# Optimization experiments

Measured on AMD Instinct MI355X. Metric: run time of the kernel, lower is better.

The kernel has to match this reference:

```python
import jax, jax.numpy as jnp
import numpy as np

B, T, D = 2, 2048, 1024
N, H = 16, 64  # num_heads, head_dim
LOG2E = 1.442695041
NEG_INF = -1.0e9


def setup_inputs() -> dict:
    key = jax.random.key(0)
    ks = jax.random.split(key, 6)
    return {
        "input_tensor": jax.random.normal(ks[0], (B, T, D), dtype=jnp.float32),
        "attention_mask": jax.random.randint(ks[1], (B, 1, T, T), 0, 2, dtype=jnp.int32),
        "wq": jax.random.normal(ks[2], (D, N, H), dtype=jnp.float32),
        "bq": jnp.zeros((N, H), dtype=jnp.float32),
        "wk": jax.random.normal(ks[3], (D, N, H), dtype=jnp.float32),
        "bk": jnp.zeros((N, H), dtype=jnp.float32),
        "wv": jax.random.normal(ks[4], (D, N, H), dtype=jnp.float32),
        "bv": jnp.zeros((N, H), dtype=jnp.float32),
        "wo": jax.random.normal(ks[5], (D, N, H), dtype=jnp.float32),
        "bo": jnp.zeros((D,), dtype=jnp.float32),
        "per_dim_scale": jnp.zeros((H,), dtype=jnp.float32),
    }


def reference(input_tensor, attention_mask, wq, bq, wk, bk, wv, bv, wo, bo, per_dim_scale):
    # QKV projections: [B,T,D] x [D,N,H] -> [B,T,N,H]
    q = jnp.einsum('btd,dnh->btnh', input_tensor, wq) + bq
    k = jnp.einsum('btd,dnh->btnh', input_tensor, wk) + bk
    v = jnp.einsum('btd,dnh->btnh', input_tensor, wv) + bv
    # per-dim query scaling: (log2(e)/sqrt(H)) * softplus(per_dim_scale)
    scale = (LOG2E / jnp.sqrt(jnp.asarray(H, q.dtype))) * jax.nn.softplus(per_dim_scale)
    q = q * scale
    # scores: [B,N,T,S]
    scores = jnp.einsum('btnh,bsnh->bnts', q, k)
    scores = jnp.where(attention_mask == 0, jnp.asarray(NEG_INF, scores.dtype), scores)
    weights = jax.nn.softmax(scores, axis=-1)
    # AV: [B,N,T,S] x [B,S,N,H] -> [B,T,N,H]
    attn_out = jnp.einsum('bnts,bsnh->btnh', weights, v)
    # output projection: [B,T,N,H] x [D,N,H] -> [B,T,D]
    return jnp.einsum('btnh,dnh->btd', attn_out, wo) + bo
```

## Files before the change

kernel.cpp:

```cpp
#include <hip/hip_runtime.h>
#include <math.h>

typedef __bf16 bf16;
typedef __attribute__((ext_vector_type(8))) __bf16 bf16x8;
typedef __attribute__((ext_vector_type(4))) __bf16 bf16x4;
typedef __attribute__((ext_vector_type(4))) float f32x4;

#define BB 2
#define TT 2048
#define DD 1024
#define NHD 16
#define HD 64
#define MM (BB*TT)
#define LOG2E_F 1.442695041f
#define NEGINF_F (-1.0e9f)

__device__ __forceinline__ void gld16(const bf16* g, bf16* l)
{
    __builtin_amdgcn_global_load_lds(
        (const __attribute__((address_space(1))) unsigned int*)g,
        (__attribute__((address_space(3))) unsigned int*)l, 16, 0, 0);
}

__global__ __launch_bounds__(256)
void prep_all(const float* __restrict__ X, const int* __restrict__ m,
              const float* __restrict__ wq, const float* __restrict__ wk,
              const float* __restrict__ wv, const float* __restrict__ wo,
              bf16* __restrict__ Xh, bf16* __restrict__ Xl,
              bf16* __restrict__ qkh, bf16* __restrict__ qkl,
              bf16* __restrict__ vh, bf16* __restrict__ ob,
              unsigned* __restrict__ bits)
{
    __shared__ float tile[32][33];
    const int bid = blockIdx.x;
    const int t   = threadIdx.x;

    if (bid < 4096) {
        int i = bid * 256 + t;
        float4 v = ((const float4*)X)[i];
        float f[4] = {v.x, v.y, v.z, v.w};
        bf16x4 h, l;
        #pragma unroll
        for (int j = 0; j < 4; ++j) {
            bf16 hh = (bf16)f[j];
            h[j] = hh;
            l[j] = (bf16)(f[j] - (float)hh);
        }
        *(bf16x4*)(Xh + (size_t)i * 4) = h;
        *(bf16x4*)(Xl + (size_t)i * 4) = l;
        return;
    }
    if (bid < 8192) {
        const int idx = bid - 4096;
        const int z   = idx >> 10;
        const int bx  = (idx & 31) << 5;
        const int by  = ((idx >> 5) & 31) << 5;
        const int r   = t >> 3;
        const int c4  = (t & 7) << 2;
        if (z == 3) {
            float4 v = *(const float4*)(wo + (size_t)(by + r) * 1024 + bx + c4);
            bf16x4 o = { (bf16)v.x, (bf16)v.y, (bf16)v.z, (bf16)v.w };
            *(bf16x4*)(ob + (size_t)(by + r) * 1024 + bx + c4) = o;
            return;
        }
        const float* src = (z == 0) ? wq : ((z == 1) ? wk : wv);
        bf16* oh = (z == 0) ? qkh : ((z == 1) ? qkh + 1048576 : vh);
        bf16* ol = (z == 0) ? qkl : ((z == 1) ? qkl + 1048576 : nullptr);
        float4 v = *(const float4*)(src + (size_t)(by + r) * 1024 + bx + c4);
        tile[r][c4+0] = v.x; tile[r][c4+1] = v.y;
        tile[r][c4+2] = v.z; tile[r][c4+3] = v.w;
        __syncthreads();
        bf16x4 hv, lv;
        #pragma unroll
        for (int j = 0; j < 4; ++j) {
            float f = tile[c4 + j][r];
            bf16 h = (bf16)f;
            hv[j] = h;
            lv[j] = (bf16)(f - (float)h);
        }
        *(bf16x4*)(oh + (size_t)(bx + r) * 1024 + by + c4) = hv;
        if (ol)
            *(bf16x4*)(ol + (size_t)(bx + r) * 1024 + by + c4) = lv;
        return;
    }
    {
        int i = (bid - 8192) * 256 + t;
        int lane = t & 63;
        int v = m[i];
        unsigned long long bl = __ballot(v != 0);
        if ((lane & 31) == 0)
            bits[i >> 5] = (unsigned)(bl >> (lane & 32));
    }
}

__global__ __launch_bounds__(256)
void gemm_qk(const bf16* __restrict__ Xh, const bf16* __restrict__ Xl,
             const bf16* __restrict__ Wh, const bf16* __restrict__ Wl,
             const float* __restrict__ bq, const float* __restrict__ bk,
             const float* __restrict__ pds,
             bf16* __restrict__ oQh, bf16* __restrict__ oQl,
             bf16* __restrict__ oKh, bf16* __restrict__ oKl)
{
    __shared__ bf16 Ah[128 * 32];
    __shared__ bf16 Al[128 * 32];
    __shared__ bf16 Bh[128 * 32];
    __shared__ bf16 Bl[128 * 32];

    const int t    = threadIdx.x;
    const int lane = t & 63;
    const int w    = t >> 6;
    const int quad = lane >> 4, l15 = lane & 15;
    const int m0   = blockIdx.y << 7;
    const int n0   = blockIdx.x << 7;
    const int wm   = (w >> 1) << 6;
    const int wn   = (w & 1)  << 6;

    const int jr0 = ((w * 2 + 0) << 4) + (lane >> 2);
    const int jr1 = ((w * 2 + 1) << 4) + (lane >> 2);
    const int kch = (lane & 3) << 3;

    bf16* lAh0 = Ah + (w * 2 + 0) * 512;  bf16* lAh1 = Ah + (w * 2 + 1) * 512;
    bf16* lAl0 = Al + (w * 2 + 0) * 512;  bf16* lAl1 = Al + (w * 2 + 1) * 512;
    bf16* lBh0 = Bh + (w * 2 + 0) * 512;  bf16* lBh1 = Bh + (w * 2 + 1) * 512;
    bf16* lBl0 = Bl + (w * 2 + 0) * 512;  bf16* lBl1 = Bl + (w * 2 + 1) * 512;

    const bf16* pAh0 = Xh + (size_t)(m0 + jr0) * DD + kch;
    const bf16* pAh1 = Xh + (size_t)(m0 + jr1) * DD + kch;
    const bf16* pAl0 = Xl + (size_t)(m0 + jr0) * DD + kch;
    const bf16* pAl1 = Xl + (size_t)(m0 + jr1) * DD + kch;
    const bf16* pBh0 = Wh + (size_t)(n0 + jr0) * DD + kch;
    const bf16* pBh1 = Wh + (size_t)(n0 + jr1) * DD + kch;
    const bf16* pBl0 = Wl + (size_t)(n0 + jr0) * DD + kch;
    const bf16* pBl1 = Wl + (size_t)(n0 + jr1) * DD + kch;

    f32x4 acc[4][4] = {};

    for (int k0 = 0; k0 < DD; k0 += 32) {
        __syncthreads();
        gld16(pAh0 + k0, lAh0);  gld16(pAh1 + k0, lAh1);
        gld16(pAl0 + k0, lAl0);  gld16(pAl1 + k0, lAl1);
        gld16(pBh0 + k0, lBh0);  gld16(pBh1 + k0, lBh1);
        gld16(pBl0 + k0, lBl0);  gld16(pBl1 + k0, lBl1);
        __syncthreads();

        bf16x8 ah[4], bh[4];
        #pragma unroll
        for (int mt = 0; mt < 4; ++mt)
            ah[mt] = *(const bf16x8*)(Ah + (wm + (mt << 4) + l15) * 32 + (quad << 3));
        #pragma unroll
        for (int nt = 0; nt < 4; ++nt)
            bh[nt] = *(const bf16x8*)(Bh + (wn + (nt << 4) + l15) * 32 + (quad << 3));
        #pragma unroll
        for (int mt = 0; mt < 4; ++mt)
            #pragma unroll
            for (int nt = 0; nt < 4; ++nt)
                acc[mt][nt] = __builtin_amdgcn_mfma_f32_16x16x32_bf16(
                    ah[mt], bh[nt], acc[mt][nt], 0, 0, 0);

        bf16x8 bl[4];
        #pragma unroll
        for (int nt = 0; nt < 4; ++nt)
            bl[nt] = *(const bf16x8*)(Bl + (wn + (nt << 4) + l15) * 32 + (quad << 3));
        #pragma unroll
        for (int mt = 0; mt < 4; ++mt)
            #pragma unroll
            for (int nt = 0; nt < 4; ++nt)
                acc[mt][nt] = __builtin_amdgcn_mfma_f32_16x16x32_bf16(
                    ah[mt], bl[nt], acc[mt][nt], 0, 0, 0);

        bf16x8 al[4];
        #pragma unroll
        for (int mt = 0; mt < 4; ++mt)
            al[mt] = *(const bf16x8*)(Al + (wm + (mt << 4) + l15) * 32 + (quad << 3));
        #pragma unroll
        for (int mt = 0; mt < 4; ++mt)
            #pragma unroll
            for (int nt = 0; nt < 4; ++nt)
                acc[mt][nt] = __builtin_amdgcn_mfma_f32_16x16x32_bf16(
                    al[mt], bh[nt], acc[mt][nt], 0, 0, 0);
    }

    #pragma unroll
    for (int nt = 0; nt < 4; ++nt) {
        const int col = n0 + wn + (nt << 4) + l15;
        const int isQ = (col < 1024);
        const int nh  = col & 1023;
        const int n   = nh >> 6, h = nh & 63;
        const float bcol = isQ ? bq[nh] : bk[nh];
        float s = 1.f;
        if (isQ) {
            float x  = pds[h];
            float sp = fmaxf(x, 0.f) + log1pf(expf(-fabsf(x)));
            s = (LOG2E_F * LOG2E_F / 8.0f) * sp;
        }
        bf16* dH = isQ ? oQh : oKh;
        bf16* dL = isQ ? oQl : oKl;
        #pragma unroll
        for (int mt = 0; mt < 4; ++mt) {
            #pragma unroll
            for (int reg = 0; reg < 4; ++reg) {
                const int row = m0 + wm + (mt << 4) + (quad << 2) + reg;
                const int bi  = row >> 11;
                const int tt  = row & (TT - 1);
                float val = (acc[mt][nt][reg] + bcol) * s;
                const size_t idx = (((size_t)bi * NHD + n) * TT + tt) * HD + h;
                bf16 hi = (bf16)val;
                dH[idx] = hi;
                dL[idx] = (bf16)(val - (float)hi);
            }
        }
    }
}

__global__ __launch_bounds__(256)
void gemm128(const bf16* __restrict__ A, const bf16* __restrict__ Bt,
             const float* __restrict__ bias,
             bf16* __restrict__ oVt, float* __restrict__ oF, const int mode)
{
    __shared__ bf16 As[128 * 32];
    __shared__ bf16 Bs[128 * 32];

    const int t    = threadIdx.x;
    const int lane = t & 63;
    const int w    = t >> 6;
    const int quad = lane >> 4, l15 = lane & 15;
    const int m0   = blockIdx.y << 7;
    const int n0   = blockIdx.x << 7;
    const int wm   = (w >> 1) << 6;
    const int wn   = (w & 1)  << 6;

    const int jr0 = ((w * 2 + 0) << 4) + (lane >> 2);
    const int jr1 = ((w * 2 + 1) << 4) + (lane >> 2);
    const int kch = (lane & 3) << 3;

    bf16* lA0 = As + (w * 2 + 0) * 512;
    bf16* lA1 = As + (w * 2 + 1) * 512;
    bf16* lB0 = Bs + (w * 2 + 0) * 512;
    bf16* lB1 = Bs + (w * 2 + 1) * 512;

    const bf16* Ap0 = A  + (size_t)(m0 + jr0) * DD + kch;
    const bf16* Ap1 = A  + (size_t)(m0 + jr1) * DD + kch;
    const bf16* Bp0 = Bt + (size_t)(n0 + jr0) * DD + kch;
    const bf16* Bp1 = Bt + (size_t)(n0 + jr1) * DD + kch;

    f32x4 acc[4][4] = {};

    for (int k0 = 0; k0 < DD; k0 += 32) {
        __syncthreads();
        gld16(Ap0 + k0, lA0);
        gld16(Ap1 + k0, lA1);
        gld16(Bp0 + k0, lB0);
        gld16(Bp1 + k0, lB1);
        __syncthreads();
        bf16x8 af[4], bfm[4];
        #pragma unroll
        for (int mt = 0; mt < 4; ++mt)
            af[mt] = *(const bf16x8*)(As + (wm + (mt << 4) + l15) * 32 + (quad << 3));
        #pragma unroll
        for (int nt = 0; nt < 4; ++nt)
            bfm[nt] = *(const bf16x8*)(Bs + (wn + (nt << 4) + l15) * 32 + (quad << 3));
        #pragma unroll
        for (int mt = 0; mt < 4; ++mt)
            #pragma unroll
            for (int nt = 0; nt < 4; ++nt)
                acc[mt][nt] = __builtin_amdgcn_mfma_f32_16x16x32_bf16(
                    af[mt], bfm[nt], acc[mt][nt], 0, 0, 0);
    }

    if (mode == 1) {
        #pragma unroll
        for (int nt = 0; nt < 4; ++nt) {
            const int col = n0 + wn + (nt << 4) + l15;
            const int bi  = col >> 11;
            const int tt  = col & (TT - 1);
            #pragma unroll
            for (int mt = 0; mt < 4; ++mt) {
                #pragma unroll
                for (int reg = 0; reg < 4; ++reg) {
                    const int row = m0 + wm + (mt << 4) + (quad << 2) + reg;
                    float val = acc[mt][nt][reg] + bias[row];
                    oVt[((size_t)bi * 1024 + row) * TT + tt] = (bf16)val;
                }
            }
        }
    } else {
        #pragma unroll
        for (int nt = 0; nt < 4; ++nt) {
            const int col = n0 + wn + (nt << 4) + l15;
            const float bcol = bias[col];
            #pragma unroll
            for (int mt = 0; mt < 4; ++mt) {
                #pragma unroll
                for (int reg = 0; reg < 4; ++reg) {
                    const int row = m0 + wm + (mt << 4) + (quad << 2) + reg;
                    oF[(size_t)row * DD + col] = acc[mt][nt][reg] + bcol;
                }
            }
        }
    }
}

__global__ __launch_bounds__(256)
void attn_mfma(const bf16* __restrict__ Qh, const bf16* __restrict__ Ql,
               const bf16* __restrict__ Kh, const bf16* __restrict__ Kl,
               const bf16* __restrict__ Vt, const unsigned* __restrict__ mbits,
               bf16* __restrict__ AO)
{
    __shared__ bf16 Ksh[64][72];
    __shared__ bf16 Ksl[64][72];
    __shared__ bf16 Vts[64][72];
    __shared__ bf16 Ps[4][16][72];
    __shared__ unsigned msk[64][2];

    const int t    = threadIdx.x;
    const int lane = t & 63;
    const int w    = t >> 6;
    const int quad = lane >> 4, l15 = lane & 15;
    const int bn   = blockIdx.y;
    const int b    = bn >> 4, n = bn & 15;
    const int q0   = blockIdx.x << 6;

    const bf16* Qbh = Qh + (size_t)bn * TT * HD;
    const bf16* Qbl = Ql + (size_t)bn * TT * HD;
    const bf16* Kbh = Kh + (size_t)bn * TT * HD;
    const bf16* Kbl = Kl + (size_t)bn * TT * HD;
    const bf16* Vtb = Vt + (size_t)bn * HD * TT;

    const int qrow = q0 + (w << 4) + l15;
    bf16x8 qfh[2], qfl[2];
    qfh[0] = *(const bf16x8*)(Qbh + (size_t)qrow * HD + (quad << 3));
    qfh[1] = *(const bf16x8*)(Qbh + (size_t)qrow * HD + 32 + (quad << 3));
    qfl[0] = *(const bf16x8*)(Qbl + (size_t)qrow * HD + (quad << 3));
    qfl[1] = *(const bf16x8*)(Qbl + (size_t)qrow * HD + 32 + (quad << 3));

    f32x4 O[4];
    #pragma unroll
    for (int i = 0; i < 4; ++i) O[i] = (f32x4){0.f,0.f,0.f,0.f};
    float m_i = -INFINITY;
    float l_i = 0.f;

    const int rS = t >> 2, cS = (t & 3) << 4;

    for (int kb = 0; kb < TT; kb += 64) {
        const bf16* kph = Kbh + (size_t)(kb + rS) * HD + cS;
        const bf16* kpl = Kbl + (size_t)(kb + rS) * HD + cS;
        bf16x8 kh0 = *(const bf16x8*)kph;
        bf16x8 kh1 = *(const bf16x8*)(kph + 8);
        bf16x8 kl0 = *(const bf16x8*)kpl;
        bf16x8 kl1 = *(const bf16x8*)(kpl + 8);
        const bf16* vp = Vtb + (size_t)rS * TT + kb + cS;
        bf16x8 v0v = *(const bf16x8*)vp;
        bf16x8 v1v = *(const bf16x8*)(vp + 8);
        unsigned mw = 0;
        if (t < 128)
            mw = mbits[((size_t)b * TT + q0 + (t >> 1)) * (TT / 32) + (kb >> 5) + (t & 1)];

        __syncthreads();
        *(bf16x8*)&Ksh[rS][cS]     = kh0;
        *(bf16x8*)&Ksh[rS][cS + 8] = kh1;
        *(bf16x8*)&Ksl[rS][cS]     = kl0;
        *(bf16x8*)&Ksl[rS][cS + 8] = kl1;
        *(bf16x8*)&Vts[rS][cS]     = v0v;
        *(bf16x8*)&Vts[rS][cS + 8] = v1v;
        if (t < 128) msk[t >> 1][t & 1] = mw;
        __syncthreads();

        f32x4 s_acc[4];
        #pragma unroll
        for (int i = 0; i < 4; ++i) s_acc[i] = (f32x4){0.f,0.f,0.f,0.f};
        #pragma unroll
        for (int k2 = 0; k2 < 2; ++k2) {
            #pragma unroll
            for (int nt = 0; nt < 4; ++nt) {
                bf16x8 bkh = *(const bf16x8*)&Ksh[(nt << 4) + l15][(k2 << 5) + (quad << 3)];
                bf16x8 bkl = *(const bf16x8*)&Ksl[(nt << 4) + l15][(k2 << 5) + (quad << 3)];
                s_acc[nt] = __builtin_amdgcn_mfma_f32_16x16x32_bf16(bkh, qfh[k2], s_acc[nt], 0, 0, 0);
                s_acc[nt] = __builtin_amdgcn_mfma_f32_16x16x32_bf16(bkl, qfh[k2], s_acc[nt], 0, 0, 0);
                s_acc[nt] = __builtin_amdgcn_mfma_f32_16x16x32_bf16(bkh, qfl[k2], s_acc[nt], 0, 0, 0);
            }
        }

        const unsigned w0 = msk[(w << 4) + l15][0];
        const unsigned w1 = msk[(w << 4) + l15][1];
        float sv[16];
        #pragma unroll
        for (int nt = 0; nt < 4; ++nt) {
            const unsigned word = (nt & 2) ? w1 : w0;
            #pragma unroll
            for (int reg = 0; reg < 4; ++reg) {
                const int bit = ((nt & 1) << 4) + (quad << 2) + reg;
                sv[nt * 4 + reg] = ((word >> bit) & 1u) ? s_acc[nt][reg] : NEGINF_F;
            }
        }
        float mx = sv[0];
        #pragma unroll
        for (int i = 1; i < 16; ++i) mx = fmaxf(mx, sv[i]);
        mx = fmaxf(mx, __shfl_xor(mx, 16));
        mx = fmaxf(mx, __shfl_xor(mx, 32));
        const float mnew  = fmaxf(m_i, mx);
        const float alpha = exp2f(m_i - mnew);
        float p[16], sum = 0.f;
        #pragma unroll
        for (int i = 0; i < 16; ++i) { p[i] = exp2f(sv[i] - mnew); sum += p[i]; }
        sum += __shfl_xor(sum, 16);
        sum += __shfl_xor(sum, 32);
        l_i = l_i * alpha + sum;
        m_i = mnew;
        #pragma unroll
        for (int nt = 0; nt < 4; ++nt) {
            O[nt][0] *= alpha; O[nt][1] *= alpha;
            O[nt][2] *= alpha; O[nt][3] *= alpha;
            bf16x4 pv = { (bf16)p[nt * 4 + 0], (bf16)p[nt * 4 + 1],
                          (bf16)p[nt * 4 + 2], (bf16)p[nt * 4 + 3] };
            *(bf16x4*)&Ps[w][l15][(nt << 4) + (quad << 2)] = pv;
        }

        #pragma unroll
        for (int s2 = 0; s2 < 2; ++s2) {
            bf16x8 ap = *(const bf16x8*)&Ps[w][l15][(s2 << 5) + (quad << 3)];
            #pragma unroll
            for (int nt = 0; nt < 4; ++nt) {
                bf16x8 bv = *(const bf16x8*)&Vts[(nt << 4) + l15][(s2 << 5) + (quad << 3)];
                O[nt] = __builtin_amdgcn_mfma_f32_16x16x32_bf16(bv, ap, O[nt], 0, 0, 0);
            }
        }
    }

    {
        const float inv = 1.0f / l_i;
        const size_t base = ((size_t)b * TT + qrow) * (NHD * HD) + (size_t)n * HD;
        #pragma unroll
        for (int nt = 0; nt < 4; ++nt) {
            bf16x4 o = { (bf16)(O[nt][0] * inv), (bf16)(O[nt][1] * inv),
                         (bf16)(O[nt][2] * inv), (bf16)(O[nt][3] * inv) };
            *(bf16x4*)(AO + base + (nt << 4) + (quad << 2)) = o;
        }
    }
}

extern "C" void kernel_launch(void* const* d_in, const int* in_sizes, int n_in,
                              void* d_out, int out_size, void* d_ws, size_t ws_size,
                              hipStream_t stream)
{
    const float* X   = (const float*)d_in[0];
    const int*   msk = (const int*)d_in[1];
    const float* wq  = (const float*)d_in[2];
    const float* bq  = (const float*)d_in[3];
    const float* wk  = (const float*)d_in[4];
    const float* bk  = (const float*)d_in[5];
    const float* wv  = (const float*)d_in[6];
    const float* bv  = (const float*)d_in[7];
    const float* wo  = (const float*)d_in[8];
    const float* bo  = (const float*)d_in[9];
    const float* pds = (const float*)d_in[10];
    float* out = (float*)d_out;

    bf16* ws   = (bf16*)d_ws;
    bf16* Xh   = ws;
    bf16* Xl   = ws + 4194304;
    bf16* WQKh = ws + 8388608;
    bf16* WQKl = ws + 10485760;
    bf16* Wvh  = ws + 12582912;
    bf16* Wob  = ws + 13631488;
    bf16* Qhb  = ws + 14680064;
    bf16* Qlb  = ws + 18874368;
    bf16* Khb  = ws + 23068672;
    bf16* Klb  = ws + 27262976;
    unsigned* mbits = (unsigned*)(ws + 31457280);
    bf16* Vtb  = Xl;
    bf16* AOb  = Xh;

    dim3 blk(256);

    prep_all<<<40960, blk, 0, stream>>>(X, msk, wq, wk, wv, wo,
                                        Xh, Xl, WQKh, WQKl, Wvh, Wob, mbits);

    gemm_qk<<<dim3(16, 32), blk, 0, stream>>>(
        Xh, Xl, WQKh, WQKl, bq, bk, pds, Qhb, Qlb, Khb, Klb);

    gemm128<<<dim3(32, 8), blk, 0, stream>>>(
        Wvh, Xh, bv, Vtb, nullptr, 1);

    dim3 ga(TT / 64, BB * NHD);
    attn_mfma<<<ga, blk, 0, stream>>>(Qhb, Qlb, Khb, Klb, Vtb, mbits, AOb);

    gemm128<<<dim3(8, 32), blk, 0, stream>>>(
        AOb, Wob, bo, nullptr, out, 2);
}
```

Measured before the change: 344.5 us.

## Merge QK and V projection launches and double attention query tile to 128

Combines the Q/K split-precision projection and the V projection into a single kernel launch dispatched by block index, writing V to a separate workspace region so the two are independent. Attention blocks now use 512 threads covering 128 query rows, halving repeated K/V and Vt tile loads per query. This trades fewer, larger attention blocks and possibly lower occupancy for less launch overhead and more shared-memory reuse.

```diff
diff --git a/kernel.cpp b/kernel.cpp
--- a/kernel.cpp
+++ b/kernel.cpp
@@ -94,17 +94,181 @@
 }
 
 __global__ __launch_bounds__(256)
-void gemm_qk(const bf16* __restrict__ Xh, const bf16* __restrict__ Xl,
-             const bf16* __restrict__ Wh, const bf16* __restrict__ Wl,
-             const float* __restrict__ bq, const float* __restrict__ bk,
-             const float* __restrict__ pds,
-             bf16* __restrict__ oQh, bf16* __restrict__ oQl,
-             bf16* __restrict__ oKh, bf16* __restrict__ oKl)
+void gemm_proj(const bf16* __restrict__ Xh, const bf16* __restrict__ Xl,
+               const bf16* __restrict__ Wh, const bf16* __restrict__ Wl,
+               const bf16* __restrict__ Wvh,
+               const float* __restrict__ bq, const float* __restrict__ bk,
+               const float* __restrict__ bv, const float* __restrict__ pds,
+               bf16* __restrict__ oQh, bf16* __restrict__ oQl,
+               bf16* __restrict__ oKh, bf16* __restrict__ oKl,
+               bf16* __restrict__ oVt)
 {
-    __shared__ bf16 Ah[128 * 32];
-    __shared__ bf16 Al[128 * 32];
-    __shared__ bf16 Bh[128 * 32];
-    __shared__ bf16 Bl[128 * 32];
+    __shared__ bf16 S[4][128 * 32];
+
+    const int bid  = blockIdx.x;
+    const int t    = threadIdx.x;
+    const int lane = t & 63;
+    const int w    = t >> 6;
+    const int quad = lane >> 4, l15 = lane & 15;
+    const int wm   = (w >> 1) << 6;
+    const int wn   = (w & 1)  << 6;
+
+    const int jr0 = ((w * 2 + 0) << 4) + (lane >> 2);
+    const int jr1 = ((w * 2 + 1) << 4) + (lane >> 2);
+    const int kch = (lane & 3) << 3;
+    const int off0 = (w * 2 + 0) * 512;
+    const int off1 = (w * 2 + 1) * 512;
+
+    if (bid < 512) {
+        const int m0 = (bid >> 4) << 7;
+        const int n0 = (bid & 15) << 7;
+        bf16* Ah = S[0]; bf16* Al = S[1]; bf16* Bh = S[2]; bf16* Bl = S[3];
+
+        const bf16* pAh0 = Xh + (size_t)(m0 + jr0) * DD + kch;
+        const bf16* pAh1 = Xh + (size_t)(m0 + jr1) * DD + kch;
+        const bf16* pAl0 = Xl + (size_t)(m0 + jr0) * DD + kch;
+        const bf16* pAl1 = Xl + (size_t)(m0 + jr1) * DD + kch;
+        const bf16* pBh0 = Wh + (size_t)(n0 + jr0) * DD + kch;
+        const bf16* pBh1 = Wh + (size_t)(n0 + jr1) * DD + kch;
+        const bf16* pBl0 = Wl + (size_t)(n0 + jr0) * DD + kch;
+        const bf16* pBl1 = Wl + (size_t)(n0 + jr1) * DD + kch;
+
+        f32x4 acc[4][4] = {};
+
+        for (int k0 = 0; k0 < DD; k0 += 32) {
+            __syncthreads();
+            gld16(pAh0 + k0, Ah + off0);  gld16(pAh1 + k0, Ah + off1);
+            gld16(pAl0 + k0, Al + off0);  gld16(pAl1 + k0, Al + off1);
+            gld16(pBh0 + k0, Bh + off0);  gld16(pBh1 + k0, Bh + off1);
+            gld16(pBl0 + k0, Bl + off0);  gld16(pBl1 + k0, Bl + off1);
+            __syncthreads();
+
+            bf16x8 ah[4], bh[4];
+            #pragma unroll
+            for (int mt = 0; mt < 4; ++mt)
+                ah[mt] = *(const bf16x8*)(Ah + (wm + (mt << 4) + l15) * 32 + (quad << 3));
+            #pragma unroll
+            for (int nt = 0; nt < 4; ++nt)
+                bh[nt] = *(const bf16x8*)(Bh + (wn + (nt << 4) + l15) * 32 + (quad << 3));
+            #pragma unroll
+            for (int mt = 0; mt < 4; ++mt)
+                #pragma unroll
+                for (int nt = 0; nt < 4; ++nt)
+                    acc[mt][nt] = __builtin_amdgcn_mfma_f32_16x16x32_bf16(
+                        ah[mt], bh[nt], acc[mt][nt], 0, 0, 0);
+
+            bf16x8 bl[4];
+            #pragma unroll
+            for (int nt = 0; nt < 4; ++nt)
+                bl[nt] = *(const bf16x8*)(Bl + (wn + (nt << 4) + l15) * 32 + (quad << 3));
+            #pragma unroll
+            for (int mt = 0; mt < 4; ++mt)
+                #pragma unroll
+                for (int nt = 0; nt < 4; ++nt)
+                    acc[mt][nt] = __builtin_amdgcn_mfma_f32_16x16x32_bf16(
+                        ah[mt], bl[nt], acc[mt][nt], 0, 0, 0);
+
+            bf16x8 al[4];
+            #pragma unroll
+            for (int mt = 0; mt < 4; ++mt)
+                al[mt] = *(const bf16x8*)(Al + (wm + (mt << 4) + l15) * 32 + (quad << 3));
+            #pragma unroll
+            for (int mt = 0; mt < 4; ++mt)
+                #pragma unroll
+                for (int nt = 0; nt < 4; ++nt)
+                    acc[mt][nt] = __builtin_amdgcn_mfma_f32_16x16x32_bf16(
+                        al[mt], bh[nt], acc[mt][nt], 0, 0, 0);
+        }
+
+        #pragma unroll
+        for (int nt = 0; nt < 4; ++nt) {
+            const int col = n0 + wn + (nt << 4) + l15;
+            const int isQ = (col < 1024);
+            const int nh  = col & 1023;
+            const int n   = nh >> 6, h = nh & 63;
+            const float bcol = isQ ? bq[nh] : bk[nh];
+            float s = 1.f;
+            if (isQ) {
+                float x  = pds[h];
+                float sp = fmaxf(x, 0.f) + log1pf(expf(-fabsf(x)));
+                s = (LOG2E_F * LOG2E_F / 8.0f) * sp;
+            }
+            bf16* dH = isQ ? oQh : oKh;
+            bf16* dL = isQ ? oQl : oKl;
+            #pragma unroll
+            for (int mt = 0; mt < 4; ++mt) {
+                #pragma unroll
+                for (int reg = 0; reg < 4; ++reg) {
+                    const int row = m0 + wm + (mt << 4) + (quad << 2) + reg;
+                    const int bi  = row >> 11;
+                    const int tt  = row & (TT - 1);
+                    float val = (acc[mt][nt][reg] + bcol) * s;
+                    const size_t idx = (((size_t)bi * NHD + n) * TT + tt) * HD + h;
+                    bf16 hi = (bf16)val;
+                    dH[idx] = hi;
+                    dL[idx] = (bf16)(val - (float)hi);
+                }
+            }
+        }
+    } else {
+        const int idx = bid - 512;
+        const int m0  = (idx >> 5) << 7;
+        const int n0  = (idx & 31) << 7;
+        bf16* As = S[0]; bf16* Bs = S[2];
+
+        const bf16* Ap0 = Wvh + (size_t)(m0 + jr0) * DD + kch;
+        const bf16* Ap1 = Wvh + (size_t)(m0 + jr1) * DD + kch;
+        const bf16* Bp0 = Xh  + (size_t)(n0 + jr0) * DD + kch;
+        const bf16* Bp1 = Xh  + (size_t)(n0 + jr1) * DD + kch;
+
+        f32x4 acc[4][4] = {};
+
+        for (int k0 = 0; k0 < DD; k0 += 32) {
+            __syncthreads();
+            gld16(Ap0 + k0, As + off0);
+            gld16(Ap1 + k0, As + off1);
+            gld16(Bp0 + k0, Bs + off0);
+            gld16(Bp1 + k0, Bs + off1);
+            __syncthreads();
+            bf16x8 af[4], bfm[4];
+            #pragma unroll
+            for (int mt = 0; mt < 4; ++mt)
+                af[mt] = *(const bf16x8*)(As + (wm + (mt << 4) + l15) * 32 + (quad << 3));
+            #pragma unroll
+            for (int nt = 0; nt < 4; ++nt)
+                bfm[nt] = *(const bf16x8*)(Bs + (wn + (nt << 4) + l15) * 32 + (quad << 3));
+            #pragma unroll
+            for (int mt = 0; mt < 4; ++mt)
+                #pragma unroll
+                for (int nt = 0; nt < 4; ++nt)
+                    acc[mt][nt] = __builtin_amdgcn_mfma_f32_16x16x32_bf16(
+                        af[mt], bfm[nt], acc[mt][nt], 0, 0, 0);
+        }
+
+        #pragma unroll
+        for (int nt = 0; nt < 4; ++nt) {
+            const int col = n0 + wn + (nt << 4) + l15;
+            const int bi  = col >> 11;
+            const int tt  = col & (TT - 1);
+            #pragma unroll
+            for (int mt = 0; mt < 4; ++mt) {
+                #pragma unroll
+                for (int reg = 0; reg < 4; ++reg) {
+                    const int row = m0 + wm + (mt << 4) + (quad << 2) + reg;
+                    float val = acc[mt][nt][reg] + bv[row];
+                    oVt[((size_t)bi * 1024 + row) * TT + tt] = (bf16)val;
+                }
+            }
+        }
+    }
+}
+
+__global__ __launch_bounds__(256)
+void gemm_out(const bf16* __restrict__ A, const bf16* __restrict__ Bt,
+              const float* __restrict__ bias, float* __restrict__ oF)
+{
+    __shared__ bf16 As[128 * 32];
+    __shared__ bf16 Bs[128 * 32];
 
     const int t    = threadIdx.x;
     const int lane = t & 63;
@@ -119,120 +283,6 @@
     const int jr1 = ((w * 2 + 1) << 4) + (lane >> 2);
     const int kch = (lane & 3) << 3;
 
-    bf16* lAh0 = Ah + (w * 2 + 0) * 512;  bf16* lAh1 = Ah + (w * 2 + 1) * 512;
-    bf16* lAl0 = Al + (w * 2 + 0) * 512;  bf16* lAl1 = Al + (w * 2 + 1) * 512;
-    bf16* lBh0 = Bh + (w * 2 + 0) * 512;  bf16* lBh1 = Bh + (w * 2 + 1) * 512;
-    bf16* lBl0 = Bl + (w * 2 + 0) * 512;  bf16* lBl1 = Bl + (w * 2 + 1) * 512;
-
-    const bf16* pAh0 = Xh + (size_t)(m0 + jr0) * DD + kch;
-    const bf16* pAh1 = Xh + (size_t)(m0 + jr1) * DD + kch;
-    const bf16* pAl0 = Xl + (size_t)(m0 + jr0) * DD + kch;
-    const bf16* pAl1 = Xl + (size_t)(m0 + jr1) * DD + kch;
-    const bf16* pBh0 = Wh + (size_t)(n0 + jr0) * DD + kch;
-    const bf16* pBh1 = Wh + (size_t)(n0 + jr1) * DD + kch;
-    const bf16* pBl0 = Wl + (size_t)(n0 + jr0) * DD + kch;
-    const bf16* pBl1 = Wl + (size_t)(n0 + jr1) * DD + kch;
-
-    f32x4 acc[4][4] = {};
-
-    for (int k0 = 0; k0 < DD; k0 += 32) {
-        __syncthreads();
-        gld16(pAh0 + k0, lAh0);  gld16(pAh1 + k0, lAh1);
-        gld16(pAl0 + k0, lAl0);  gld16(pAl1 + k0, lAl1);
-        gld16(pBh0 + k0, lBh0);  gld16(pBh1 + k0, lBh1);
-        gld16(pBl0 + k0, lBl0);  gld16(pBl1 + k0, lBl1);
-        __syncthreads();
-
-        bf16x8 ah[4], bh[4];
-        #pragma unroll
-        for (int mt = 0; mt < 4; ++mt)
-            ah[mt] = *(const bf16x8*)(Ah + (wm + (mt << 4) + l15) * 32 + (quad << 3));
-        #pragma unroll
-        for (int nt = 0; nt < 4; ++nt)
-            bh[nt] = *(const bf16x8*)(Bh + (wn + (nt << 4) + l15) * 32 + (quad << 3));
-        #pragma unroll
-        for (int mt = 0; mt < 4; ++mt)
-            #pragma unroll
-            for (int nt = 0; nt < 4; ++nt)
-                acc[mt][nt] = __builtin_amdgcn_mfma_f32_16x16x32_bf16(
-                    ah[mt], bh[nt], acc[mt][nt], 0, 0, 0);
-
-        bf16x8 bl[4];
-        #pragma unroll
-        for (int nt = 0; nt < 4; ++nt)
-            bl[nt] = *(const bf16x8*)(Bl + (wn + (nt << 4) + l15) * 32 + (quad << 3));
-        #pragma unroll
-        for (int mt = 0; mt < 4; ++mt)
-            #pragma unroll
-            for (int nt = 0; nt < 4; ++nt)
-                acc[mt][nt] = __builtin_amdgcn_mfma_f32_16x16x32_bf16(
-                    ah[mt], bl[nt], acc[mt][nt], 0, 0, 0);
-
-        bf16x8 al[4];
-        #pragma unroll
-        for (int mt = 0; mt < 4; ++mt)
-            al[mt] = *(const bf16x8*)(Al + (wm + (mt << 4) + l15) * 32 + (quad << 3));
-        #pragma unroll
-        for (int mt = 0; mt < 4; ++mt)
-            #pragma unroll
-            for (int nt = 0; nt < 4; ++nt)
-                acc[mt][nt] = __builtin_amdgcn_mfma_f32_16x16x32_bf16(
-                    al[mt], bh[nt], acc[mt][nt], 0, 0, 0);
-    }
-
-    #pragma unroll
-    for (int nt = 0; nt < 4; ++nt) {
-        const int col = n0 + wn + (nt << 4) + l15;
-        const int isQ = (col < 1024);
-        const int nh  = col & 1023;
-        const int n   = nh >> 6, h = nh & 63;
-        const float bcol = isQ ? bq[nh] : bk[nh];
-        float s = 1.f;
-        if (isQ) {
-            float x  = pds[h];
-            float sp = fmaxf(x, 0.f) + log1pf(expf(-fabsf(x)));
-            s = (LOG2E_F * LOG2E_F / 8.0f) * sp;
-        }
-        bf16* dH = isQ ? oQh : oKh;
-        bf16* dL = isQ ? oQl : oKl;
-        #pragma unroll
-        for (int mt = 0; mt < 4; ++mt) {
-            #pragma unroll
-            for (int reg = 0; reg < 4; ++reg) {
-                const int row = m0 + wm + (mt << 4) + (quad << 2) + reg;
-                const int bi  = row >> 11;
-                const int tt  = row & (TT - 1);
-                float val = (acc[mt][nt][reg] + bcol) * s;
-                const size_t idx = (((size_t)bi * NHD + n) * TT + tt) * HD + h;
-                bf16 hi = (bf16)val;
-                dH[idx] = hi;
-                dL[idx] = (bf16)(val - (float)hi);
-            }
-        }
-    }
-}
-
-__global__ __launch_bounds__(256)
-void gemm128(const bf16* __restrict__ A, const bf16* __restrict__ Bt,
-             const float* __restrict__ bias,
-             bf16* __restrict__ oVt, float* __restrict__ oF, const int mode)
-{
-    __shared__ bf16 As[128 * 32];
-    __shared__ bf16 Bs[128 * 32];
-
-    const int t    = threadIdx.x;
-    const int lane = t & 63;
-    const int w    = t >> 6;
-    const int quad = lane >> 4, l15 = lane & 15;
-    const int m0   = blockIdx.y << 7;
-    const int n0   = blockIdx.x << 7;
-    const int wm   = (w >> 1) << 6;
-    const int wn   = (w & 1)  << 6;
-
-    const int jr0 = ((w * 2 + 0) << 4) + (lane >> 2);
-    const int jr1 = ((w * 2 + 1) << 4) + (lane >> 2);
-    const int kch = (lane & 3) << 3;
-
     bf16* lA0 = As + (w * 2 + 0) * 512;
     bf16* lA1 = As + (w * 2 + 1) * 512;
     bf16* lB0 = Bs + (w * 2 + 0) * 512;
@@ -267,40 +317,22 @@
                     af[mt], bfm[nt], acc[mt][nt], 0, 0, 0);
     }
 
-    if (mode == 1) {
-        #pragma unroll
-        for (int nt = 0; nt < 4; ++nt) {
-            const int col = n0 + wn + (nt << 4) + l15;
-            const int bi  = col >> 11;
-            const int tt  = col & (TT - 1);
-            #pragma unroll
-            for (int mt = 0; mt < 4; ++mt) {
-                #pragma unroll
-                for (int reg = 0; reg < 4; ++reg) {
-                    const int row = m0 + wm + (mt << 4) + (quad << 2) + reg;
-                    float val = acc[mt][nt][reg] + bias[row];
-                    oVt[((size_t)bi * 1024 + row) * TT + tt] = (bf16)val;
-                }
-            }
-        }
-    } else {
-        #pragma unroll
-        for (int nt = 0; nt < 4; ++nt) {
-            const int col = n0 + wn + (nt << 4) + l15;
-            const float bcol = bias[col];
-            #pragma unroll
-            for (int mt = 0; mt < 4; ++mt) {
-                #pragma unroll
-                for (int reg = 0; reg < 4; ++reg) {
-                    const int row = m0 + wm + (mt << 4) + (quad << 2) + reg;
-                    oF[(size_t)row * DD + col] = acc[mt][nt][reg] + bcol;
-                }
+    #pragma unroll
+    for (int nt = 0; nt < 4; ++nt) {
+        const int col = n0 + wn + (nt << 4) + l15;
+        const float bcol = bias[col];
+        #pragma unroll
+        for (int mt = 0; mt < 4; ++mt) {
+            #pragma unroll
+            for (int reg = 0; reg < 4; ++reg) {
+                const int row = m0 + wm + (mt << 4) + (quad << 2) + reg;
+                oF[(size_t)row * DD + col] = acc[mt][nt][reg] + bcol;
             }
         }
     }
 }
 
-__global__ __launch_bounds__(256)
+__global__ __launch_bounds__(512)
 void attn_mfma(const bf16* __restrict__ Qh, const bf16* __restrict__ Ql,
                const bf16* __restrict__ Kh, const bf16* __restrict__ Kl,
                const bf16* __restrict__ Vt, const unsigned* __restrict__ mbits,
@@ -309,8 +341,8 @@
     __shared__ bf16 Ksh[64][72];
     __shared__ bf16 Ksl[64][72];
     __shared__ bf16 Vts[64][72];
-    __shared__ bf16 Ps[4][16][72];
-    __shared__ unsigned msk[64][2];
+    __shared__ bf16 Ps[8][16][72];
+    __shared__ unsigned msk[128][2];
 
     const int t    = threadIdx.x;
     const int lane = t & 63;
@@ -318,7 +350,7 @@
     const int quad = lane >> 4, l15 = lane & 15;
     const int bn   = blockIdx.y;
     const int b    = bn >> 4, n = bn & 15;
-    const int q0   = blockIdx.x << 6;
+    const int q0   = blockIdx.x << 7;
 
     const bf16* Qbh = Qh + (size_t)bn * TT * HD;
     const bf16* Qbl = Ql + (size_t)bn * TT * HD;
@@ -339,30 +371,21 @@
     float m_i = -INFINITY;
     float l_i = 0.f;
 
-    const int rS = t >> 2, cS = (t & 3) << 4;
+    const int rS = t >> 3, cS = (t & 7) << 3;
 
     for (int kb = 0; kb < TT; kb += 64) {
-        const bf16* kph = Kbh + (size_t)(kb + rS) * HD + cS;
-        const bf16* kpl = Kbl + (size_t)(kb + rS) * HD + cS;
-        bf16x8 kh0 = *(const bf16x8*)kph;
-        bf16x8 kh1 = *(const bf16x8*)(kph + 8);
-        bf16x8 kl0 = *(const bf16x8*)kpl;
-        bf16x8 kl1 = *(const bf16x8*)(kpl + 8);
-        const bf16* vp = Vtb + (size_t)rS * TT + kb + cS;
-        bf16x8 v0v = *(const bf16x8*)vp;
-        bf16x8 v1v = *(const bf16x8*)(vp + 8);
+        bf16x8 khv = *(const bf16x8*)(Kbh + (size_t)(kb + rS) * HD + cS);
+        bf16x8 klv = *(const bf16x8*)(Kbl + (size_t)(kb + rS) * HD + cS);
+        bf16x8 vv  = *(const bf16x8*)(Vtb + (size_t)rS * TT + kb + cS);
         unsigned mw = 0;
-        if (t < 128)
+        if (t < 256)
             mw = mbits[((size_t)b * TT + q0 + (t >> 1)) * (TT / 32) + (kb >> 5) + (t & 1)];
 
         __syncthreads();
-        *(bf16x8*)&Ksh[rS][cS]     = kh0;
-        *(bf16x8*)&Ksh[rS][cS + 8] = kh1;
-        *(bf16x8*)&Ksl[rS][cS]     = kl0;
-        *(bf16x8*)&Ksl[rS][cS + 8] = kl1;
-        *(bf16x8*)&Vts[rS][cS]     = v0v;
-        *(bf16x8*)&Vts[rS][cS + 8] = v1v;
-        if (t < 128) msk[t >> 1][t & 1] = mw;
+        *(bf16x8*)&Ksh[rS][cS] = khv;
+        *(bf16x8*)&Ksl[rS][cS] = klv;
+        *(bf16x8*)&Vts[rS][cS] = vv;
+        if (t < 256) msk[t >> 1][t & 1] = mw;
         __syncthreads();
 
         f32x4 s_acc[4];
@@ -475,15 +498,13 @@
     prep_all<<<40960, blk, 0, stream>>>(X, msk, wq, wk, wv, wo,
                                         Xh, Xl, WQKh, WQKl, Wvh, Wob, mbits);
 
-    gemm_qk<<<dim3(16, 32), blk, 0, stream>>>(
-        Xh, Xl, WQKh, WQKl, bq, bk, pds, Qhb, Qlb, Khb, Klb);
-
-    gemm128<<<dim3(32, 8), blk, 0, stream>>>(
-        Wvh, Xh, bv, Vtb, nullptr, 1);
-
-    dim3 ga(TT / 64, BB * NHD);
-    attn_mfma<<<ga, blk, 0, stream>>>(Qhb, Qlb, Khb, Klb, Vtb, mbits, AOb);
-
-    gemm128<<<dim3(8, 32), blk, 0, stream>>>(
-        AOb, Wob, bo, nullptr, out, 2);
+    gemm_proj<<<768, blk, 0, stream>>>(
+        Xh, Xl, WQKh, WQKl, Wvh, bq, bk, bv, pds,
+        Qhb, Qlb, Khb, Klb, (bf16*)(ws + 32505856));
+
+    dim3 ga(TT / 128, BB * NHD);
+    attn_mfma<<<ga, dim3(512), 0, stream>>>(
+        Qhb, Qlb, Khb, Klb, (bf16*)(ws + 32505856), mbits, AOb);
+
+    gemm_out<<<dim3(8, 32), blk, 0, stream>>>(AOb, Wob, bo, out);
 }
```

Measured after the change: 319.4 us. -7.3%, faster.
